# Kernel tuning notes

Hardware: AMD Instinct MI355X
Metric: run time of the kernel (lower is better)

## Reference

```python
import jax, jax.numpy as jnp
import numpy as np
from jax.scipy.special import logsumexp

B, T, V, E, F, H, L = 64, 512, 30000, 256, 256, 256, 9
DROPOUT_RATE, DROPOUT_ROUND = 0.1, 4


def setup_inputs() -> dict:
    key = jax.random.key(0)
    ks = jax.random.split(key, 20)
    lengths = jax.random.randint(ks[0], (B,), T // 2, T + 1)
    tok = jax.random.randint(ks[1], (B, T), 1, V)
    input_ids = jnp.where(jnp.arange(T)[None, :] < lengths[:, None], tok, 0).astype(jnp.int32)
    labels = jax.random.randint(ks[2], (B, T), 0, L).astype(jnp.int32)
    W_emb = (jax.random.normal(ks[3], (V, E)) * 0.1).at[0].set(0.0)  # padding_idx=0 row zeroed
    w0 = jax.random.normal(ks[4], (F, F, 3)) * 0.05
    w1 = jax.random.normal(ks[5], (F, F, 3)) * 0.05
    w2 = jax.random.normal(ks[6], (F, F, 3)) * 0.05
    Wl = jax.random.normal(ks[7], (E, F)) * 0.05
    Wh = jax.random.normal(ks[8], (F, H)) * 0.05
    Wfc = jax.random.normal(ks[9], (H, L)) * 0.05
    crf_start = jax.random.normal(ks[10], (L,)) * 0.1
    crf_end = jax.random.normal(ks[11], (L,)) * 0.1
    crf_trans = jax.random.normal(ks[12], (L, L)) * 0.1
    z = jnp.zeros
    return dict(input_ids=input_ids, labels=labels, W_emb=W_emb,
                w0=w0, b0=z((F,)), w1=w1, b1=z((F,)), w2=w2, b2=z((F,)),
                Wl=Wl, bl=z((F,)), Wh=Wh, bh=z((H,)), Wfc=Wfc, bfc=z((L,)),
                crf_start=crf_start, crf_end=crf_end, crf_trans=crf_trans)


def _conv1d(x, w, b, dil):
    # x: [B, C, T]; w: [O, I, K]; 'same' padding given kernel 3 / dilation
    pad = 1 + dil - 1  # kernel_size//2 + dilation - 1
    y = jax.lax.conv_general_dilated(x, w, window_strides=(1,), padding=[(pad, pad)],
                                     rhs_dilation=(dil,), dimension_numbers=('NCH', 'OIH', 'NCH'))
    return y + b[None, :, None]


def reference(input_ids, labels, W_emb, w0, b0, w1, b1, w2, b2,
              Wl, bl, Wh, bh, Wfc, bfc, crf_start, crf_end, crf_trans):
    mask = input_ids > 0  # [B,T] bool, mask[:,0] all True by construction

    # --- encoder: embedding + IDCNN ---
    emb = W_emb[input_ids]                       # [B,T,E]
    x = (emb @ Wl + bl).transpose(0, 2, 1)       # [B,F,T]

    def block(h):  # faithful to add_module name collision: conv0 -> relu -> conv1 -> conv2
        h = _conv1d(h, w0, b0, 1)
        h = jax.nn.relu(h)
        h = _conv1d(h, w1, b1, 1)
        h = _conv1d(h, w2, b2, 2)
        return h

    x = block(x)
    x = jax.nn.relu(x)
    x = block(x)
    x = block(x)
    x = block(x)

    out = x.transpose(0, 2, 1) @ Wh + bh         # [B,T,H]

    # --- multisample dropout + fc (deterministic masks via fixed keys) ---
    keep = 1.0 - DROPOUT_RATE
    logits = jnp.zeros((B, T, L), dtype=out.dtype)
    for r in range(DROPOUT_ROUND):
        m = jax.random.bernoulli(jax.random.fold_in(jax.random.key(42), r), keep, out.shape)
        logits = logits + ((out * m / keep) @ Wfc + bfc)
    logits = logits / DROPOUT_ROUND              # [B,T,L] emissions

    # --- CRF negative log-likelihood (reduction='sum') ---
    fmask = mask.astype(logits.dtype)

    # numerator: score of gold path
    emit_sc = jnp.take_along_axis(logits, labels[..., None], axis=-1)[..., 0]  # [B,T]
    trans_sc = crf_trans[labels[:, :-1], labels[:, 1:]]                        # [B,T-1]
    numer = crf_start[labels[:, 0]] + emit_sc[:, 0]
    numer = numer + jnp.sum((trans_sc + emit_sc[:, 1:]) * fmask[:, 1:], axis=1)
    seq_ends = jnp.sum(mask, axis=1).astype(jnp.int32) - 1
    last_tags = labels[jnp.arange(B), seq_ends]
    numer = numer + crf_end[last_tags]

    # denominator: forward algorithm (sequential scan over time)
    alpha0 = crf_start[None, :] + logits[:, 0]   # [B,L]

    def step(alpha, xs):
        em_t, m_t = xs                            # [B,L], [B]
        nxt = logsumexp(alpha[:, :, None] + crf_trans[None] + em_t[:, None, :], axis=1)
        alpha = jnp.where(m_t[:, None], nxt, alpha)
        return alpha, None

    alpha, _ = jax.lax.scan(step, alpha0, (logits[:, 1:].transpose(1, 0, 2), mask[:, 1:].T))
    denom = logsumexp(alpha + crf_end[None, :], axis=1)

    loss = jnp.sum(denom - numer)  # = -crf.llh(sum)
    return loss
```

## Files before the change

### kernel.cpp

```cpp
#include <hip/hip_runtime.h>
#include <stdint.h>

#define B_ 64
#define T_ 512
#define V_ 30000
#define E_ 256
#define F_ 256
#define H_ 256
#define L_ 9
#define TP_ 516
#define M_ (B_*T_)
#define HALF_ ((B_*T_*H_)/2)
#define NCHUNK_ 64

typedef float f32x4 __attribute__((ext_vector_type(4)));
typedef __bf16 bf16x8 __attribute__((ext_vector_type(8)));

typedef __attribute__((address_space(3))) unsigned int lds_uint;
typedef __attribute__((address_space(1))) const unsigned int glob_uint;

__device__ __forceinline__ unsigned short f2b(float f) {
  unsigned u = __float_as_uint(f);
  unsigned r = (u + 0x7FFFu + ((u >> 16) & 1u)) >> 16;
  return (unsigned short)r;
}
__device__ __forceinline__ unsigned pack2(float a, float b) {
  return (unsigned)f2b(a) | ((unsigned)f2b(b) << 16);
}

__device__ __forceinline__ void threefry2x32(unsigned k0, unsigned k1,
                                             unsigned x0, unsigned x1,
                                             unsigned &o0, unsigned &o1) {
  unsigned ks2 = k0 ^ k1 ^ 0x1BD11BDAu;
  x0 += k0; x1 += k1;
#define TFR(r) { x0 += x1; x1 = (x1 << r) | (x1 >> (32 - r)); x1 ^= x0; }
  TFR(13) TFR(15) TFR(26) TFR(6)   x0 += k1;  x1 += ks2 + 1u;
  TFR(17) TFR(29) TFR(16) TFR(24)  x0 += ks2; x1 += k0 + 2u;
  TFR(13) TFR(15) TFR(26) TFR(6)   x0 += k0;  x1 += k1 + 3u;
  TFR(17) TFR(29) TFR(16) TFR(24)  x0 += k1;  x1 += ks2 + 4u;
  TFR(13) TFR(15) TFR(26) TFR(6)   x0 += ks2; x1 += k0 + 5u;
#undef TFR
  o0 = x0; o1 = x1;
}

__global__ __launch_bounds__(256) void zero_pads(unsigned short* xb0, unsigned short* xb1) {
  int idx = blockIdx.x * 256 + threadIdx.x;
  int b = idx >> 10, rr = (idx >> 8) & 3, f = idx & 255;
  int row = (rr < 2) ? rr : 512 + rr;
  int o = (b * TP_ + row) * 256 + f;
  xb0[o] = 0; xb1[o] = 0;
}

__global__ __launch_bounds__(256) void prep_convw(const float* __restrict__ w,
                                                  unsigned short* __restrict__ BT) {
  int idx = blockIdx.x * 256 + threadIdx.x;
  if (idx < F_ * 768) {
    int o = idx / 768;
    int rem = idx - o * 768;
    int kk = rem >> 8;
    int i = rem & 255;
    BT[idx] = f2b(w[(o * 256 + i) * 3 + kk]);
  }
}

__global__ __launch_bounds__(256) void prep_mat(const float* __restrict__ Wm,
                                                unsigned short* __restrict__ BT) {
  int idx = blockIdx.x * 256 + threadIdx.x;
  int f = idx >> 8, e = idx & 255;
  BT[idx] = f2b(Wm[e * 256 + f]);
}

__global__ void foldkeys(unsigned* fk) {
  if (threadIdx.x == 0 && blockIdx.x == 0) {
    for (int r = 0; r < 4; ++r) {
      unsigned o0, o1;
      threefry2x32(0u, 42u, 0u, (unsigned)r, o0, o1);
      fk[2 * r] = o0; fk[2 * r + 1] = o1;
    }
  }
}

__global__ __launch_bounds__(256) void dropout_mask(const unsigned* __restrict__ fkg,
                                                    unsigned char* __restrict__ cnt) {
  unsigned fk0[4], fk1[4];
#pragma unroll
  for (int r = 0; r < 4; ++r) { fk0[r] = fkg[2 * r]; fk1[r] = fkg[2 * r + 1]; }
  const unsigned j0 = (blockIdx.x * 256 + threadIdx.x) * 4;
  unsigned c0 = 0, c1 = 0;
#pragma unroll
  for (int e = 0; e < 4; ++e) {
    unsigned a = 0, b = 0;
#pragma unroll
    for (int r = 0; r < 4; ++r) {
      unsigned o0, o1;
      threefry2x32(fk0[r], fk1[r], j0 + e, j0 + e + (unsigned)HALF_, o0, o1);
      a += (o0 < 0xE6666600u) ? 1u : 0u;
      b += (o1 < 0xE6666600u) ? 1u : 0u;
    }
    c0 |= a << (8 * e);
    c1 |= b << (8 * e);
  }
  *(unsigned*)(cnt + j0) = c0;
  *(unsigned*)(cnt + HALF_ + j0) = c1;
}

template<int DIL, bool RELU>
__global__ __launch_bounds__(256, 2)
void conv3_gemm(const unsigned short* __restrict__ xin,
                const unsigned short* __restrict__ BT,
                const float* __restrict__ bias,
                unsigned short* __restrict__ xout) {
  __shared__ unsigned short Al[132 * 32];
  __shared__ unsigned short Bl[3 * 128 * 32];
  const int tid = threadIdx.x;
  const int tm = blockIdx.x, tn = blockIdx.y;
  const int lane = tid & 63, wid = tid >> 6;
  const int wm = wid >> 1, wn = wid & 1;
  const int fr = lane & 15, fq = lane >> 4;

  const int r0 = tm * 128;
  const int bb0 = r0 >> 9, t0 = r0 & 511;
  const int pb = bb0 * TP_ + t0;

  int aoff[2];
#pragma unroll
  for (int s = 0; s < 2; ++s) {
    int c = s * 256 + tid;
    aoff[s] = (pb + (c >> 2)) * 256 + (c & 3) * 8;
  }
  const int hoff = (pb + 128 + (tid >> 2)) * 256 + (tid & 3) * 8;
  int boff[6];
#pragma unroll
  for (int s = 0; s < 6; ++s) {
    int c = s * 256 + tid;
    boff[s] = (tn * 128 + ((c >> 2) & 127)) * 768 + (c >> 9) * 256 + (c & 3) * 8;
  }
  unsigned short* abase[2];
  unsigned short* bbase[6];
#pragma unroll
  for (int s = 0; s < 2; ++s) abase[s] = Al + (s * 256 + wid * 64) * 8;
#pragma unroll
  for (int s = 0; s < 6; ++s) bbase[s] = Bl + (s * 256 + wid * 64) * 8;

  f32x4 acc[4][4] = {};

  for (int kin = 0; kin < 256; kin += 32) {
#pragma unroll
    for (int s = 0; s < 2; ++s)
      __builtin_amdgcn_global_load_lds((glob_uint*)(xin + aoff[s] + kin),
                                       (lds_uint*)(abase[s]), 16, 0, 0);
#pragma unroll
    for (int s = 0; s < 6; ++s)
      __builtin_amdgcn_global_load_lds((glob_uint*)(BT + boff[s] + kin),
                                       (lds_uint*)(bbase[s]), 16, 0, 0);
    if (tid < 16) {
      uint4 v = *(const uint4*)(xin + hoff + kin);
      *(uint4*)(&Al[(128 + (tid >> 2)) * 32 + (tid & 3) * 8]) = v;
    }
    __syncthreads();
#pragma unroll
    for (int tp = 0; tp < 3; ++tp) {
      const int sh = (tp - 1) * DIL;
      bf16x8 af[4], bfv[4];
#pragma unroll
      for (int m = 0; m < 4; ++m)
        af[m] = *(const bf16x8*)(&Al[(wm * 64 + m * 16 + fr + 2 + sh) * 32 + fq * 8]);
#pragma unroll
      for (int n = 0; n < 4; ++n)
        bfv[n] = *(const bf16x8*)(&Bl[(tp * 128 + wn * 64 + n * 16 + fr) * 32 + fq * 8]);
#pragma unroll
      for (int m = 0; m < 4; ++m)
#pragma unroll
        for (int n = 0; n < 4; ++n)
          acc[m][n] = __builtin_amdgcn_mfma_f32_16x16x32_bf16(af[m], bfv[n], acc[m][n], 0, 0, 0);
    }
    __syncthreads();
  }

#pragma unroll
  for (int n = 0; n < 4; ++n) {
    const int col = tn * 128 + wn * 64 + n * 16 + fr;
    const float bs = bias[col];
#pragma unroll
    for (int m = 0; m < 4; ++m) {
      const int row0 = tm * 128 + wm * 64 + m * 16 + fq * 4;
#pragma unroll
      for (int rg = 0; rg < 4; ++rg) {
        const int row = row0 + rg;
        float x = acc[m][n][rg] + bs;
        if (RELU) x = fmaxf(x, 0.f);
        int bb = row >> 9, t = row & 511;
        xout[(bb * TP_ + t + 2) * 256 + col] = f2b(x);
      }
    }
  }
}

__global__ __launch_bounds__(256, 2)
void head_lin(const unsigned short* __restrict__ xin,
              const unsigned short* __restrict__ BTh,
              const float* __restrict__ bh,
              unsigned short* __restrict__ outh) {
  __shared__ unsigned short Al[128 * 32];
  __shared__ unsigned short Bl[128 * 32];
  const int tid = threadIdx.x;
  const int tm = blockIdx.x, tn = blockIdx.y;
  const int lane = tid & 63, wid = tid >> 6;
  const int wm = wid >> 1, wn = wid & 1;
  const int fr = lane & 15, fq = lane >> 4;

  int aoff[2], boff[2];
#pragma unroll
  for (int s = 0; s < 2; ++s) {
    int c = s * 256 + tid;
    int rr = c >> 2, q = c & 3;
    int r = tm * 128 + rr;
    aoff[s] = ((r >> 9) * TP_ + (r & 511) + 2) * 256 + q * 8;
    boff[s] = (tn * 128 + rr) * 256 + q * 8;
  }
  unsigned short *ab[2], *bb[2];
#pragma unroll
  for (int s = 0; s < 2; ++s) {
    ab[s] = Al + (s * 256 + wid * 64) * 8;
    bb[s] = Bl + (s * 256 + wid * 64) * 8;
  }

  f32x4 acc[4][4] = {};

  for (int kin = 0; kin < 256; kin += 32) {
#pragma unroll
    for (int s = 0; s < 2; ++s) {
      __builtin_amdgcn_global_load_lds((glob_uint*)(xin + aoff[s] + kin),
                                       (lds_uint*)(ab[s]), 16, 0, 0);
      __builtin_amdgcn_global_load_lds((glob_uint*)(BTh + boff[s] + kin),
                                       (lds_uint*)(bb[s]), 16, 0, 0);
    }
    __syncthreads();
    bf16x8 af[4], bfv[4];
#pragma unroll
    for (int m = 0; m < 4; ++m)
      af[m] = *(const bf16x8*)(&Al[(wm * 64 + m * 16 + fr) * 32 + fq * 8]);
#pragma unroll
    for (int n = 0; n < 4; ++n)
      bfv[n] = *(const bf16x8*)(&Bl[(wn * 64 + n * 16 + fr) * 32 + fq * 8]);
#pragma unroll
    for (int m = 0; m < 4; ++m)
#pragma unroll
      for (int n = 0; n < 4; ++n)
        acc[m][n] = __builtin_amdgcn_mfma_f32_16x16x32_bf16(af[m], bfv[n], acc[m][n], 0, 0, 0);
    __syncthreads();
  }

#pragma unroll
  for (int n = 0; n < 4; ++n) {
    const int col = tn * 128 + wn * 64 + n * 16 + fr;
    const float bs = bh[col];
#pragma unroll
    for (int m = 0; m < 4; ++m) {
      const int row0 = tm * 128 + wm * 64 + m * 16 + fq * 4;
#pragma unroll
      for (int rg = 0; rg < 4; ++rg)
        outh[(size_t)(row0 + rg) * H_ + col] = f2b(acc[m][n][rg] + bs);
    }
  }
}

__global__ __launch_bounds__(256) void head_apply(const unsigned short* __restrict__ outh,
                                                  const unsigned char* __restrict__ cnt,
                                                  const float* __restrict__ Wfc,
                                                  const float* __restrict__ bfc,
                                                  float* __restrict__ logits) {
  __shared__ float sW[H_ * L_];
  __shared__ float sB[L_];
  int tid = threadIdx.x;
  for (int i = tid; i < H_ * L_; i += 256) sW[i] = Wfc[i];
  if (tid < L_) sB[tid] = bfc[tid];
  __syncthreads();
  const int lane = tid & 63, wid = tid >> 6;
  const int fr = lane & 15, g16 = lane >> 4;
  const int row = blockIdx.x * 16 + wid * 4 + g16;
  const unsigned short* orow = outh + (size_t)row * 256 + fr * 16;
  const unsigned char* crow = cnt + (size_t)row * 256 + fr * 16;
  uint4 ob0 = *(const uint4*)orow;
  uint4 ob1 = *(const uint4*)(orow + 8);
  uint4 cb = *(const uint4*)crow;
  const float sc = 1.0f / 3.6f;
  float a[9] = {};
#pragma unroll
  for (int q = 0; q < 4; ++q) {
    unsigned w0 = (q < 2) ? ((const unsigned*)&ob0)[2 * q]     : ((const unsigned*)&ob1)[2 * (q - 2)];
    unsigned w1 = (q < 2) ? ((const unsigned*)&ob0)[2 * q + 1] : ((const unsigned*)&ob1)[2 * (q - 2) + 1];
    unsigned cw = ((const unsigned*)&cb)[q];
    float xs[4];
    xs[0] = __uint_as_float(w0 << 16);
    xs[1] = __uint_as_float(w0 & 0xFFFF0000u);
    xs[2] = __uint_as_float(w1 << 16);
    xs[3] = __uint_as_float(w1 & 0xFFFF0000u);
#pragma unroll
    for (int k = 0; k < 4; ++k) {
      const int h = fr * 16 + q * 4 + k;
      const float x = xs[k] * (float)((cw >> (8 * k)) & 255u) * sc;
#pragma unroll
      for (int c = 0; c < 9; ++c) a[c] = fmaf(x, sW[h * 9 + c], a[c]);
    }
  }
#pragma unroll
  for (int c = 0; c < 9; ++c)
#pragma unroll
    for (int o = 1; o < 16; o <<= 1) a[c] += __shfl_xor(a[c], o);
  if (fr == 0) {
#pragma unroll
    for (int c = 0; c < 9; ++c) logits[(size_t)row * 9 + c] = a[c] + sB[c];
  }
}

__global__ __launch_bounds__(256) void crf_numer(const int* __restrict__ ids,
                                                 const int* __restrict__ labels,
                                                 const float* __restrict__ logits,
                                                 const float* __restrict__ cstart,
                                                 const float* __restrict__ cend,
                                                 const float* __restrict__ ctrans,
                                                 float* __restrict__ numer) {
  int b = blockIdx.x, tid = threadIdx.x;
  __shared__ float rs[256];
  __shared__ int rc[256];
  float p = 0.f; int cnt = 0;
  for (int t = tid; t < T_; t += 256) {
    int lab = labels[b * T_ + t];
    float em = logits[(b * T_ + t) * L_ + lab];
    int mk = ids[b * T_ + t] > 0;
    cnt += mk;
    if (t == 0) {
      p += cstart[lab] + em;
    } else if (mk) {
      int lp = labels[b * T_ + t - 1];
      p += ctrans[lp * L_ + lab] + em;
    }
  }
  rs[tid] = p; rc[tid] = cnt;
  __syncthreads();
  for (int s = 128; s > 0; s >>= 1) {
    if (tid < s) { rs[tid] += rs[tid + s]; rc[tid] += rc[tid + s]; }
    __syncthreads();
  }
  if (tid == 0) {
    int se = rc[0] - 1;
    int lt = labels[b * T_ + se];
    numer[b] = rs[0] + cend[lt];
  }
}

__global__ __launch_bounds__(128) void crf_chunk(const int* __restrict__ ids,
                                                 const float* __restrict__ logits,
                                                 const float* __restrict__ ctrans,
                                                 float* __restrict__ mats) {
  int blk = blockIdx.x;
  int b = blk >> 6, c = blk & 63;
  int e = threadIdx.x;
  int i = e / 9, j = e - 9 * i;
  __shared__ float cur[81];
  __shared__ float em[8 * 9];
  __shared__ int mk[8];
  int t0 = 8 * c;
  if (e < 72) em[e] = logits[((size_t)b * T_ + t0) * L_ + e];
  if (e < 8) mk[e] = (t0 + e >= 1) ? (ids[b * T_ + t0 + e] > 0) : 0;
  bool act = e < 81;
  float tcol[9];
  if (act) {
#pragma unroll
    for (int k = 0; k < 9; ++k) tcol[k] = ctrans[k * 9 + j];
    cur[e] = (i == j) ? 0.f : -1e30f;
  }
  __syncthreads();
  for (int s = 0; s < 8; ++s) {
    if (mk[s]) {
      float nv = 0.f;
      if (act) {
        float vv[9], mx = -3e38f;
#pragma unroll
        for (int k = 0; k < 9; ++k) { vv[k] = cur[i * 9 + k] + tcol[k]; mx = fmaxf(mx, vv[k]); }
        float ss = 0.f;
#pragma unroll
        for (int k = 0; k < 9; ++k) ss += __expf(vv[k] - mx);
        nv = mx + __logf(ss) + em[s * 9 + j];
      }
      __syncthreads();
      if (act) cur[e] = nv;
      __syncthreads();
    }
  }
  if (act) mats[(size_t)blk * 81 + e] = cur[e];
}

__global__ __launch_bounds__(256) void crf_combine(const float* __restrict__ mats,
                                                   const float* __restrict__ logits,
                                                   const float* __restrict__ cstart,
                                                   const float* __restrict__ cend,
                                                   const float* __restrict__ numer,
                                                   float* __restrict__ parts) {
  int b = blockIdx.x;
  __shared__ float bufA[64 * 81];
  __shared__ float bufB[32 * 81];
  __shared__ float alphaT[L_];
  int tid = threadIdx.x;
  for (int x = tid; x < 64 * 81; x += 256) bufA[x] = mats[(size_t)b * 64 * 81 + x];
  __syncthreads();
  float* src = bufA;
  float* dst = bufB;
  for (int n = 32; n >= 1; n >>= 1) {
    for (int x = tid; x < n * 81; x += 256) {
      int p = x / 81, e = x - 81 * p;
      int i = e / 9, j = e - 9 * i;
      const float* Lm = src + 162 * p;
      const float* Rm = Lm + 81;
      float vv[9], mx = -3e38f;
#pragma unroll
      for (int k = 0; k < 9; ++k) { vv[k] = Lm[i * 9 + k] + Rm[k * 9 + j]; mx = fmaxf(mx, vv[k]); }
      float ss = 0.f;
#pragma unroll
      for (int k = 0; k < 9; ++k) ss += __expf(vv[k] - mx);
      dst[x] = mx + __logf(ss);
    }
    __syncthreads();
    float* tmp = src; src = dst; dst = tmp;
  }
  const float* M = src;
  if (tid < L_) {
    int j = tid;
    float vv[9], mx = -3e38f;
#pragma unroll
    for (int i = 0; i < 9; ++i) {
      float a0 = cstart[i] + logits[(size_t)b * T_ * L_ + i];
      vv[i] = a0 + M[i * 9 + j];
      mx = fmaxf(mx, vv[i]);
    }
    float ss = 0.f;
#pragma unroll
    for (int i = 0; i < 9; ++i) ss += __expf(vv[i] - mx);
    alphaT[j] = mx + __logf(ss) + cend[j];
  }
  __syncthreads();
  if (tid == 0) {
    float mx = -3e38f;
#pragma unroll
    for (int j = 0; j < 9; ++j) mx = fmaxf(mx, alphaT[j]);
    float ss = 0.f;
#pragma unroll
    for (int j = 0; j < 9; ++j) ss += __expf(alphaT[j] - mx);
    parts[b] = mx + __logf(ss) - numer[b];
  }
}

__global__ void final_reduce(const float* __restrict__ parts, float* __restrict__ out) {
  int tid = threadIdx.x;
  float v = parts[tid];
#pragma unroll
  for (int off = 32; off; off >>= 1) v += __shfl_down(v, off);
  if (tid == 0) out[0] = v;
}

__global__ __launch_bounds__(256, 2)
void embed_gemm(const int* __restrict__ ids,
                const float* __restrict__ Wemb,
                const unsigned short* __restrict__ BT,
                const float* __restrict__ bias,
                unsigned short* __restrict__ xout) {
  __shared__ unsigned short Al[128 * 40];
  __shared__ unsigned short Bl[128 * 40];
  const int tid = threadIdx.x;
  const int tm = blockIdx.x, tn = blockIdx.y;
  const int lane = tid & 63, wid = tid >> 6;
  const int wm = wid >> 1, wn = wid & 1;
  const int fr = lane & 15, fq = lane >> 4;

  int asrc[2], boff[2], loff[2];
#pragma unroll
  for (int it = 0; it < 2; ++it) {
    int e = it * 256 + tid;
    int row = e >> 2, kq = e & 3;
    int r = tm * 128 + row;
    asrc[it] = ids[r] * E_ + kq * 8;
    boff[it] = (tn * 128 + row) * E_ + kq * 8;
    loff[it] = row * 40 + kq * 8;
  }

  f32x4 acc[4][4] = {};

  for (int k0 = 0; k0 < E_; k0 += 32) {
#pragma unroll
    for (int it = 0; it < 2; ++it) {
      const float* s = Wemb + asrc[it] + k0;
      float4 v0 = *(const float4*)s;
      float4 v1 = *(const float4*)(s + 4);
      uint4 va;
      va.x = pack2(v0.x, v0.y); va.y = pack2(v0.z, v0.w);
      va.z = pack2(v1.x, v1.y); va.w = pack2(v1.z, v1.w);
      uint4 vb = *(const uint4*)(BT + boff[it] + k0);
      *(uint4*)(&Al[loff[it]]) = va;
      *(uint4*)(&Bl[loff[it]]) = vb;
    }
    __syncthreads();
    bf16x8 af[4], bfv[4];
#pragma unroll
    for (int m = 0; m < 4; ++m)
      af[m] = *(const bf16x8*)(&Al[(wm * 64 + m * 16 + fr) * 40 + fq * 8]);
#pragma unroll
    for (int n = 0; n < 4; ++n)
      bfv[n] = *(const bf16x8*)(&Bl[(wn * 64 + n * 16 + fr) * 40 + fq * 8]);
#pragma unroll
    for (int m = 0; m < 4; ++m)
#pragma unroll
      for (int n = 0; n < 4; ++n)
        acc[m][n] = __builtin_amdgcn_mfma_f32_16x16x32_bf16(af[m], bfv[n], acc[m][n], 0, 0, 0);
    __syncthreads();
  }

#pragma unroll
  for (int n = 0; n < 4; ++n) {
    const int col = tn * 128 + wn * 64 + n * 16 + fr;
    const float bs = bias[col];
#pragma unroll
    for (int m = 0; m < 4; ++m) {
      const int row0 = tm * 128 + wm * 64 + m * 16 + fq * 4;
#pragma unroll
      for (int rg = 0; rg < 4; ++rg) {
        const int row = row0 + rg;
        float x = acc[m][n][rg] + bs;
        int bb = row >> 9, t = row & 511;
        xout[(bb * TP_ + t + 2) * 256 + col] = f2b(x);
      }
    }
  }
}

extern "C" void kernel_launch(void* const* d_in, const int* in_sizes, int n_in,
                              void* d_out, int out_size, void* d_ws, size_t ws_size,
                              hipStream_t stream) {
  const int*   ids    = (const int*)d_in[0];
  const int*   labels = (const int*)d_in[1];
  const float* Wemb   = (const float*)d_in[2];
  const float* w0     = (const float*)d_in[3];
  const float* b0     = (const float*)d_in[4];
  const float* w1     = (const float*)d_in[5];
  const float* b1     = (const float*)d_in[6];
  const float* w2     = (const float*)d_in[7];
  const float* b2     = (const float*)d_in[8];
  const float* Wl     = (const float*)d_in[9];
  const float* bl     = (const float*)d_in[10];
  const float* Wh     = (const float*)d_in[11];
  const float* bh     = (const float*)d_in[12];
  const float* Wfc    = (const float*)d_in[13];
  const float* bfc    = (const float*)d_in[14];
  const float* cstart = (const float*)d_in[15];
  const float* cend   = (const float*)d_in[16];
  const float* ctrans = (const float*)d_in[17];

  char* ws = (char*)d_ws;
  size_t off = 0;
  auto alloc = [&](size_t bytes) -> void* {
    void* p = ws + off;
    off += (bytes + 255) & ~(size_t)255;
    return p;
  };
  unsigned short* xb0 = (unsigned short*)alloc((size_t)B_ * TP_ * F_ * 2);
  unsigned short* xb1 = (unsigned short*)alloc((size_t)B_ * TP_ * F_ * 2);
  unsigned short* BTl = (unsigned short*)alloc((size_t)E_ * F_ * 2);
  unsigned short* BT0 = (unsigned short*)alloc((size_t)F_ * 768 * 2);
  unsigned short* BT1 = (unsigned short*)alloc((size_t)F_ * 768 * 2);
  unsigned short* BT2 = (unsigned short*)alloc((size_t)F_ * 768 * 2);
  unsigned short* BTh = (unsigned short*)alloc((size_t)F_ * H_ * 2);
  unsigned short* outh = (unsigned short*)alloc((size_t)M_ * H_ * 2);
  unsigned char* cntb = (unsigned char*)alloc((size_t)M_ * H_);
  float* logits = (float*)alloc((size_t)M_ * L_ * 4);
  unsigned* fk  = (unsigned*)alloc(64);
  float* numer  = (float*)alloc(B_ * 4);
  float* parts  = (float*)alloc(B_ * 4);
  float* mats   = (float*)alloc((size_t)B_ * NCHUNK_ * 81 * 4);
  if (ws_size < off) return;

  zero_pads<<<256, 256, 0, stream>>>(xb0, xb1);
  prep_convw<<<768, 256, 0, stream>>>(w0, BT0);
  prep_convw<<<768, 256, 0, stream>>>(w1, BT1);
  prep_convw<<<768, 256, 0, stream>>>(w2, BT2);
  prep_mat<<<256, 256, 0, stream>>>(Wl, BTl);
  prep_mat<<<256, 256, 0, stream>>>(Wh, BTh);
  foldkeys<<<1, 64, 0, stream>>>(fk);
  dropout_mask<<<HALF_ / 1024, 256, 0, stream>>>(fk, cntb);

  dim3 grid(M_ / 128, F_ / 128);
  embed_gemm<<<grid, 256, 0, stream>>>(ids, Wemb, BTl, bl, xb0);

  conv3_gemm<1, true ><<<grid, 256, 0, stream>>>(xb0, BT0, b0, xb1);
  conv3_gemm<1, false><<<grid, 256, 0, stream>>>(xb1, BT1, b1, xb0);
  conv3_gemm<2, true ><<<grid, 256, 0, stream>>>(xb0, BT2, b2, xb1);
  conv3_gemm<1, true ><<<grid, 256, 0, stream>>>(xb1, BT0, b0, xb0);
  conv3_gemm<1, false><<<grid, 256, 0, stream>>>(xb0, BT1, b1, xb1);
  conv3_gemm<2, false><<<grid, 256, 0, stream>>>(xb1, BT2, b2, xb0);
  conv3_gemm<1, true ><<<grid, 256, 0, stream>>>(xb0, BT0, b0, xb1);
  conv3_gemm<1, false><<<grid, 256, 0, stream>>>(xb1, BT1, b1, xb0);
  conv3_gemm<2, false><<<grid, 256, 0, stream>>>(xb0, BT2, b2, xb1);
  conv3_gemm<1, true ><<<grid, 256, 0, stream>>>(xb1, BT0, b0, xb0);
  conv3_gemm<1, false><<<grid, 256, 0, stream>>>(xb0, BT1, b1, xb1);
  conv3_gemm<2, false><<<grid, 256, 0, stream>>>(xb1, BT2, b2, xb0);

  head_lin<<<grid, 256, 0, stream>>>(xb0, BTh, bh, outh);
  head_apply<<<M_ / 16, 256, 0, stream>>>(outh, cntb, Wfc, bfc, logits);

  crf_numer<<<B_, 256, 0, stream>>>(ids, labels, logits, cstart, cend, ctrans, numer);
  crf_chunk<<<B_ * NCHUNK_, 128, 0, stream>>>(ids, logits, ctrans, mats);
  crf_combine<<<B_, 256, 0, stream>>>(mats, logits, cstart, cend, numer, parts);
  final_reduce<<<1, 64, 0, stream>>>(parts, (float*)d_out);
}
```

Before: 354.9 us.

## Fold embedding projection into first conv and head linear into last conv

Precomputes combined weights Wl·w0 and w2·Wh, plus matching biases with edge-aware handling for the zero-padded timesteps. This removes the separate embedding GEMM and head linear GEMM, and a simple bf16 gather of embeddings replaces the embedding GEMM. The cost is extra small weight-folding prep kernels, which use naive serial loops. Numerics change slightly because rounding happens at a different point.

```diff
diff --git a/kernel.cpp b/kernel.cpp
--- a/kernel.cpp
+++ b/kernel.cpp
@@ -51,6 +51,22 @@
   xb0[o] = 0; xb1[o] = 0;
 }
 
+__global__ __launch_bounds__(256) void gather_emb(const int* __restrict__ ids,
+                                                  const float* __restrict__ Wemb,
+                                                  unsigned short* __restrict__ xb) {
+  int idx = blockIdx.x * 256 + threadIdx.x;
+  int r = idx >> 5;
+  int e0 = (idx & 31) * 8;
+  int b = r >> 9, t = r & 511;
+  const float* s = Wemb + (size_t)ids[r] * E_ + e0;
+  float4 v0 = *(const float4*)s;
+  float4 v1 = *(const float4*)(s + 4);
+  uint4 va;
+  va.x = pack2(v0.x, v0.y); va.y = pack2(v0.z, v0.w);
+  va.z = pack2(v1.x, v1.y); va.w = pack2(v1.z, v1.w);
+  *(uint4*)(xb + ((size_t)(b * TP_ + t + 2)) * 256 + e0) = va;
+}
+
 __global__ __launch_bounds__(256) void prep_convw(const float* __restrict__ w,
                                                   unsigned short* __restrict__ BT) {
   int idx = blockIdx.x * 256 + threadIdx.x;
@@ -63,11 +79,53 @@
   }
 }
 
-__global__ __launch_bounds__(256) void prep_mat(const float* __restrict__ Wm,
-                                                unsigned short* __restrict__ BT) {
-  int idx = blockIdx.x * 256 + threadIdx.x;
-  int f = idx >> 8, e = idx & 255;
-  BT[idx] = f2b(Wm[e * 256 + f]);
+__global__ __launch_bounds__(256) void prep_L1(const float* __restrict__ w0,
+                                               const float* __restrict__ Wl,
+                                               unsigned short* __restrict__ BT) {
+  int o = blockIdx.x & 255, kk = blockIdx.x >> 8;
+  int e = threadIdx.x;
+  float s = 0.f;
+  for (int i = 0; i < 256; ++i)
+    s = fmaf(w0[(o * 256 + i) * 3 + kk], Wl[e * 256 + i], s);
+  BT[o * 768 + kk * 256 + e] = f2b(s);
+}
+
+__global__ __launch_bounds__(256) void prep_L6(const float* __restrict__ w2,
+                                               const float* __restrict__ Wh,
+                                               unsigned short* __restrict__ BT) {
+  int i = blockIdx.x & 255, kk = blockIdx.x >> 8;
+  int h = threadIdx.x;
+  float s = 0.f;
+  for (int f = 0; f < 256; ++f)
+    s = fmaf(Wh[f * 256 + h], w2[(f * 256 + i) * 3 + kk], s);
+  BT[h * 768 + kk * 256 + i] = f2b(s);
+}
+
+__global__ __launch_bounds__(256) void prep_biasA(const float* __restrict__ w0,
+                                                  const float* __restrict__ bl,
+                                                  float* __restrict__ part) {
+  int kk = blockIdx.x;
+  int o = threadIdx.x;
+  float s = 0.f;
+  for (int i = 0; i < 256; ++i) s = fmaf(w0[(o * 256 + i) * 3 + kk], bl[i], s);
+  part[kk * 256 + o] = s;
+}
+
+__global__ __launch_bounds__(256) void prep_biasB(const float* __restrict__ part,
+                                                  const float* __restrict__ b0,
+                                                  const float* __restrict__ Wh,
+                                                  const float* __restrict__ b2,
+                                                  const float* __restrict__ bh,
+                                                  float* __restrict__ biasL1,
+                                                  float* __restrict__ biasL6) {
+  int o = threadIdx.x;
+  float s0 = part[o], s1 = part[256 + o], s2 = part[512 + o];
+  biasL1[o]       = b0[o] + s1 + s2;
+  biasL1[256 + o] = b0[o] + s0 + s1 + s2;
+  biasL1[512 + o] = b0[o] + s0 + s1;
+  float s = 0.f;
+  for (int f = 0; f < 256; ++f) s = fmaf(Wh[f * 256 + o], b2[f], s);
+  biasL6[o] = s + bh[o];
 }
 
 __global__ void foldkeys(unsigned* fk) {
@@ -104,7 +162,7 @@
   *(unsigned*)(cnt + HALF_ + j0) = c1;
 }
 
-template<int DIL, bool RELU>
+template<int DIL, bool RELU, bool EDGEB, bool PLAINOUT>
 __global__ __launch_bounds__(256, 2)
 void conv3_gemm(const unsigned short* __restrict__ xin,
                 const unsigned short* __restrict__ BT,
@@ -180,87 +238,27 @@
 #pragma unroll
   for (int n = 0; n < 4; ++n) {
     const int col = tn * 128 + wn * 64 + n * 16 + fr;
-    const float bs = bias[col];
+    float bs0 = 0.f, bs, bs2 = 0.f;
+    if (EDGEB) { bs0 = bias[col]; bs = bias[256 + col]; bs2 = bias[512 + col]; }
+    else bs = bias[col];
 #pragma unroll
     for (int m = 0; m < 4; ++m) {
       const int row0 = tm * 128 + wm * 64 + m * 16 + fq * 4;
 #pragma unroll
       for (int rg = 0; rg < 4; ++rg) {
         const int row = row0 + rg;
-        float x = acc[m][n][rg] + bs;
+        const int t = row & 511;
+        float bb = bs;
+        if (EDGEB) bb = (t == 0) ? bs0 : ((t == 511) ? bs2 : bs);
+        float x = acc[m][n][rg] + bb;
         if (RELU) x = fmaxf(x, 0.f);
-        int bb = row >> 9, t = row & 511;
-        xout[(bb * TP_ + t + 2) * 256 + col] = f2b(x);
+        if (PLAINOUT) {
+          xout[(size_t)row * 256 + col] = f2b(x);
+        } else {
+          int bbk = row >> 9;
+          xout[(bbk * TP_ + t + 2) * 256 + col] = f2b(x);
+        }
       }
-    }
-  }
-}
-
-__global__ __launch_bounds__(256, 2)
-void head_lin(const unsigned short* __restrict__ xin,
-              const unsigned short* __restrict__ BTh,
-              const float* __restrict__ bh,
-              unsigned short* __restrict__ outh) {
-  __shared__ unsigned short Al[128 * 32];
-  __shared__ unsigned short Bl[128 * 32];
-  const int tid = threadIdx.x;
-  const int tm = blockIdx.x, tn = blockIdx.y;
-  const int lane = tid & 63, wid = tid >> 6;
-  const int wm = wid >> 1, wn = wid & 1;
-  const int fr = lane & 15, fq = lane >> 4;
-
-  int aoff[2], boff[2];
-#pragma unroll
-  for (int s = 0; s < 2; ++s) {
-    int c = s * 256 + tid;
-    int rr = c >> 2, q = c & 3;
-    int r = tm * 128 + rr;
-    aoff[s] = ((r >> 9) * TP_ + (r & 511) + 2) * 256 + q * 8;
-    boff[s] = (tn * 128 + rr) * 256 + q * 8;
-  }
-  unsigned short *ab[2], *bb[2];
-#pragma unroll
-  for (int s = 0; s < 2; ++s) {
-    ab[s] = Al + (s * 256 + wid * 64) * 8;
-    bb[s] = Bl + (s * 256 + wid * 64) * 8;
-  }
-
-  f32x4 acc[4][4] = {};
-
-  for (int kin = 0; kin < 256; kin += 32) {
-#pragma unroll
-    for (int s = 0; s < 2; ++s) {
-      __builtin_amdgcn_global_load_lds((glob_uint*)(xin + aoff[s] + kin),
-                                       (lds_uint*)(ab[s]), 16, 0, 0);
-      __builtin_amdgcn_global_load_lds((glob_uint*)(BTh + boff[s] + kin),
-                                       (lds_uint*)(bb[s]), 16, 0, 0);
-    }
-    __syncthreads();
-    bf16x8 af[4], bfv[4];
-#pragma unroll
-    for (int m = 0; m < 4; ++m)
-      af[m] = *(const bf16x8*)(&Al[(wm * 64 + m * 16 + fr) * 32 + fq * 8]);
-#pragma unroll
-    for (int n = 0; n < 4; ++n)
-      bfv[n] = *(const bf16x8*)(&Bl[(wn * 64 + n * 16 + fr) * 32 + fq * 8]);
-#pragma unroll
-    for (int m = 0; m < 4; ++m)
-#pragma unroll
-      for (int n = 0; n < 4; ++n)
-        acc[m][n] = __builtin_amdgcn_mfma_f32_16x16x32_bf16(af[m], bfv[n], acc[m][n], 0, 0, 0);
-    __syncthreads();
-  }
-
-#pragma unroll
-  for (int n = 0; n < 4; ++n) {
-    const int col = tn * 128 + wn * 64 + n * 16 + fr;
-    const float bs = bh[col];
-#pragma unroll
-    for (int m = 0; m < 4; ++m) {
-      const int row0 = tm * 128 + wm * 64 + m * 16 + fq * 4;
-#pragma unroll
-      for (int rg = 0; rg < 4; ++rg)
-        outh[(size_t)(row0 + rg) * H_ + col] = f2b(acc[m][n][rg] + bs);
     }
   }
 }
@@ -459,80 +457,6 @@
   if (tid == 0) out[0] = v;
 }
 
-__global__ __launch_bounds__(256, 2)
-void embed_gemm(const int* __restrict__ ids,
-                const float* __restrict__ Wemb,
-                const unsigned short* __restrict__ BT,
-                const float* __restrict__ bias,
-                unsigned short* __restrict__ xout) {
-  __shared__ unsigned short Al[128 * 40];
-  __shared__ unsigned short Bl[128 * 40];
-  const int tid = threadIdx.x;
-  const int tm = blockIdx.x, tn = blockIdx.y;
-  const int lane = tid & 63, wid = tid >> 6;
-  const int wm = wid >> 1, wn = wid & 1;
-  const int fr = lane & 15, fq = lane >> 4;
-
-  int asrc[2], boff[2], loff[2];
-#pragma unroll
-  for (int it = 0; it < 2; ++it) {
-    int e = it * 256 + tid;
-    int row = e >> 2, kq = e & 3;
-    int r = tm * 128 + row;
-    asrc[it] = ids[r] * E_ + kq * 8;
-    boff[it] = (tn * 128 + row) * E_ + kq * 8;
-    loff[it] = row * 40 + kq * 8;
-  }
-
-  f32x4 acc[4][4] = {};
-
-  for (int k0 = 0; k0 < E_; k0 += 32) {
-#pragma unroll
-    for (int it = 0; it < 2; ++it) {
-      const float* s = Wemb + asrc[it] + k0;
-      float4 v0 = *(const float4*)s;
-      float4 v1 = *(const float4*)(s + 4);
-      uint4 va;
-      va.x = pack2(v0.x, v0.y); va.y = pack2(v0.z, v0.w);
-      va.z = pack2(v1.x, v1.y); va.w = pack2(v1.z, v1.w);
-      uint4 vb = *(const uint4*)(BT + boff[it] + k0);
-      *(uint4*)(&Al[loff[it]]) = va;
-      *(uint4*)(&Bl[loff[it]]) = vb;
-    }
-    __syncthreads();
-    bf16x8 af[4], bfv[4];
-#pragma unroll
-    for (int m = 0; m < 4; ++m)
-      af[m] = *(const bf16x8*)(&Al[(wm * 64 + m * 16 + fr) * 40 + fq * 8]);
-#pragma unroll
-    for (int n = 0; n < 4; ++n)
-      bfv[n] = *(const bf16x8*)(&Bl[(wn * 64 + n * 16 + fr) * 40 + fq * 8]);
-#pragma unroll
-    for (int m = 0; m < 4; ++m)
-#pragma unroll
-      for (int n = 0; n < 4; ++n)
-        acc[m][n] = __builtin_amdgcn_mfma_f32_16x16x32_bf16(af[m], bfv[n], acc[m][n], 0, 0, 0);
-    __syncthreads();
-  }
-
-#pragma unroll
-  for (int n = 0; n < 4; ++n) {
-    const int col = tn * 128 + wn * 64 + n * 16 + fr;
-    const float bs = bias[col];
-#pragma unroll
-    for (int m = 0; m < 4; ++m) {
-      const int row0 = tm * 128 + wm * 64 + m * 16 + fq * 4;
-#pragma unroll
-      for (int rg = 0; rg < 4; ++rg) {
-        const int row = row0 + rg;
-        float x = acc[m][n][rg] + bs;
-        int bb = row >> 9, t = row & 511;
-        xout[(bb * TP_ + t + 2) * 256 + col] = f2b(x);
-      }
-    }
-  }
-}
-
 extern "C" void kernel_launch(void* const* d_in, const int* in_sizes, int n_in,
                               void* d_out, int out_size, void* d_ws, size_t ws_size,
                               hipStream_t stream) {
@@ -562,13 +486,16 @@
     off += (bytes + 255) & ~(size_t)255;
     return p;
   };
-  unsigned short* xb0 = (unsigned short*)alloc((size_t)B_ * TP_ * F_ * 2);
-  unsigned short* xb1 = (unsigned short*)alloc((size_t)B_ * TP_ * F_ * 2);
-  unsigned short* BTl = (unsigned short*)alloc((size_t)E_ * F_ * 2);
-  unsigned short* BT0 = (unsigned short*)alloc((size_t)F_ * 768 * 2);
-  unsigned short* BT1 = (unsigned short*)alloc((size_t)F_ * 768 * 2);
-  unsigned short* BT2 = (unsigned short*)alloc((size_t)F_ * 768 * 2);
-  unsigned short* BTh = (unsigned short*)alloc((size_t)F_ * H_ * 2);
+  unsigned short* xb0  = (unsigned short*)alloc((size_t)B_ * TP_ * F_ * 2);
+  unsigned short* xb1  = (unsigned short*)alloc((size_t)B_ * TP_ * F_ * 2);
+  unsigned short* BT0  = (unsigned short*)alloc((size_t)F_ * 768 * 2);
+  unsigned short* BT1  = (unsigned short*)alloc((size_t)F_ * 768 * 2);
+  unsigned short* BT2  = (unsigned short*)alloc((size_t)F_ * 768 * 2);
+  unsigned short* BTL1 = (unsigned short*)alloc((size_t)F_ * 768 * 2);
+  unsigned short* BTL6 = (unsigned short*)alloc((size_t)H_ * 768 * 2);
+  float* bpart  = (float*)alloc(3 * 256 * 4);
+  float* biasL1 = (float*)alloc(3 * 256 * 4);
+  float* biasL6 = (float*)alloc(256 * 4);
   unsigned short* outh = (unsigned short*)alloc((size_t)M_ * H_ * 2);
   unsigned char* cntb = (unsigned char*)alloc((size_t)M_ * H_);
   float* logits = (float*)alloc((size_t)M_ * L_ * 4);
@@ -579,31 +506,31 @@
   if (ws_size < off) return;
 
   zero_pads<<<256, 256, 0, stream>>>(xb0, xb1);
+  gather_emb<<<4096, 256, 0, stream>>>(ids, Wemb, xb0);
   prep_convw<<<768, 256, 0, stream>>>(w0, BT0);
   prep_convw<<<768, 256, 0, stream>>>(w1, BT1);
   prep_convw<<<768, 256, 0, stream>>>(w2, BT2);
-  prep_mat<<<256, 256, 0, stream>>>(Wl, BTl);
-  prep_mat<<<256, 256, 0, stream>>>(Wh, BTh);
+  prep_L1<<<768, 256, 0, stream>>>(w0, Wl, BTL1);
+  prep_L6<<<768, 256, 0, stream>>>(w2, Wh, BTL6);
+  prep_biasA<<<3, 256, 0, stream>>>(w0, bl, bpart);
+  prep_biasB<<<1, 256, 0, stream>>>(bpart, b0, Wh, b2, bh, biasL1, biasL6);
   foldkeys<<<1, 64, 0, stream>>>(fk);
   dropout_mask<<<HALF_ / 1024, 256, 0, stream>>>(fk, cntb);
 
   dim3 grid(M_ / 128, F_ / 128);
-  embed_gemm<<<grid, 256, 0, stream>>>(ids, Wemb, BTl, bl, xb0);
-
-  conv3_gemm<1, true ><<<grid, 256, 0, stream>>>(xb0, BT0, b0, xb1);
-  conv3_gemm<1, false><<<grid, 256, 0, stream>>>(xb1, BT1, b1, xb0);
-  conv3_gemm<2, true ><<<grid, 256, 0, stream>>>(xb0, BT2, b2, xb1);
-  conv3_gemm<1, true ><<<grid, 256, 0, stream>>>(xb1, BT0, b0, xb0);
-  conv3_gemm<1, false><<<grid, 256, 0, stream>>>(xb0, BT1, b1, xb1);
-  conv3_gemm<2, false><<<grid, 256, 0, stream>>>(xb1, BT2, b2, xb0);
-  conv3_gemm<1, true ><<<grid, 256, 0, stream>>>(xb0, BT0, b0, xb1);
-  conv3_gemm<1, false><<<grid, 256, 0, stream>>>(xb1, BT1, b1, xb0);
-  conv3_gemm<2, false><<<grid, 256, 0, stream>>>(xb0, BT2, b2, xb1);
-  conv3_gemm<1, true ><<<grid, 256, 0, stream>>>(xb1, BT0, b0, xb0);
-  conv3_gemm<1, false><<<grid, 256, 0, stream>>>(xb0, BT1, b1, xb1);
-  conv3_gemm<2, false><<<grid, 256, 0, stream>>>(xb1, BT2, b2, xb0);
-
-  head_lin<<<grid, 256, 0, stream>>>(xb0, BTh, bh, outh);
+  conv3_gemm<1, true , true , false><<<grid, 256, 0, stream>>>(xb0, BTL1, biasL1, xb1);
+  conv3_gemm<1, false, false, false><<<grid, 256, 0, stream>>>(xb1, BT1, b1, xb0);
+  conv3_gemm<2, true , false, false><<<grid, 256, 0, stream>>>(xb0, BT2, b2, xb1);
+  conv3_gemm<1, true , false, false><<<grid, 256, 0, stream>>>(xb1, BT0, b0, xb0);
+  conv3_gemm<1, false, false, false><<<grid, 256, 0, stream>>>(xb0, BT1, b1, xb1);
+  conv3_gemm<2, false, false, false><<<grid, 256, 0, stream>>>(xb1, BT2, b2, xb0);
+  conv3_gemm<1, true , false, false><<<grid, 256, 0, stream>>>(xb0, BT0, b0, xb1);
+  conv3_gemm<1, false, false, false><<<grid, 256, 0, stream>>>(xb1, BT1, b1, xb0);
+  conv3_gemm<2, false, false, false><<<grid, 256, 0, stream>>>(xb0, BT2, b2, xb1);
+  conv3_gemm<1, true , false, false><<<grid, 256, 0, stream>>>(xb1, BT0, b0, xb0);
+  conv3_gemm<1, false, false, false><<<grid, 256, 0, stream>>>(xb0, BT1, b1, xb1);
+  conv3_gemm<2, false, false, true ><<<grid, 256, 0, stream>>>(xb1, BTL6, biasL6, outh);
+
   head_apply<<<M_ / 16, 256, 0, stream>>>(outh, cntb, Wfc, bfc, logits);
 
   crf_numer<<<B_, 256, 0, stream>>>(ids, labels, logits, cstart, cend, ctrans, numer);
```

Measured after the change: 409.7 us. +15.4%, slower.
